# Kernel tuning notes

Measured on AMD Instinct MI355X. Metric: run time of the kernel, lower is better.

Reference implementation:

```python
import jax, jax.numpy as jnp
import numpy as np
from jax import lax

C = 128
HEADS = 4
WS = 7      # spatial search window (per side radius 3)
WT = 1      # temporal radius -> frames t-1..t+1
EPS = 1e-6

_R = WS // 2
OFFS = np.array([(dt, dh, dw)
                 for dt in range(-WT, WT + 1)
                 for dh in range(-_R, _R + 1)
                 for dw in range(-_R, _R + 1)], dtype=np.int32)  # [L,3]


def layernorm_c(x, g, b):
    # LayerNorm2D: normalize over channel dim of [B,T,C,H,W]
    mu = jnp.mean(x, axis=2, keepdims=True)
    var = jnp.var(x, axis=2, keepdims=True)
    xn = (x - mu) * lax.rsqrt(var + EPS)
    return xn * g[None, None, :, None, None] + b[None, None, :, None, None]


def conv2d(x, w, b):
    y = lax.conv_general_dilated(x, w, (1, 1), 'SAME',
                                 dimension_numbers=('NCHW', 'OIHW', 'NCHW'))
    return y + b[None, :, None, None]


def setup_inputs() -> dict:
    key = jax.random.key(0)
    ks = jax.random.split(key, 16)
    B, T, H, W = 1, 4, 128, 128
    vid = jax.random.normal(ks[0], (B, T, C, H, W), jnp.float32)
    flows = jax.random.normal(ks[1], (B, T, 2, H, W), jnp.float32)
    s = 1.0 / np.sqrt(C)
    Wq = jax.random.normal(ks[2], (C, C), jnp.float32) * s
    Wk = jax.random.normal(ks[3], (C, C), jnp.float32) * s
    Wv = jax.random.normal(ks[4], (C, C), jnp.float32) * s
    Wo = jax.random.normal(ks[5], (C, C), jnp.float32) * s
    g0 = jnp.ones((C,), jnp.float32); b0 = jnp.zeros((C,), jnp.float32)
    g1 = jnp.ones((C,), jnp.float32); b1 = jnp.zeros((C,), jnp.float32)
    sc = 1.0 / np.sqrt(C * 9)
    w_r1 = jax.random.normal(ks[6], (C, C, 3, 3), jnp.float32) * sc
    b_r1 = jnp.zeros((C,), jnp.float32)
    w_r2 = jax.random.normal(ks[7], (C, C, 3, 3), jnp.float32) * sc
    b_r2 = jnp.zeros((C,), jnp.float32)
    return dict(vid=vid, flows=flows, g0=g0, b0=b0, Wq=Wq, Wk=Wk, Wv=Wv, Wo=Wo,
                g1=g1, b1=b1, w_r1=w_r1, b_r1=b_r1, w_r2=w_r2, b_r2=b_r2)


def _forward(vid, flows, g0, b0, Wq, Wk, Wv, Wo, g1, b1, w_r1, b_r1, w_r2, b_r2):
    B, T, _, H, W = vid.shape
    hd = C // HEADS
    N = T * H * W
    scale = hd ** -0.5

    x = layernorm_c(vid, g0, b0)
    q = jnp.einsum('btchw,oc->btohw', x, Wq)
    k = jnp.einsum('btchw,oc->btohw', x, Wk)
    v = jnp.einsum('btchw,oc->btohw', x, Wv)
    qh = q.transpose(0, 1, 3, 4, 2).reshape(B, N, HEADS, hd)
    kf = k.transpose(0, 1, 3, 4, 2).reshape(B, N, C)
    vf = v.transpose(0, 1, 3, 4, 2).reshape(B, N, C)

    tt = jnp.arange(T)[:, None, None]
    hh = jnp.arange(H)[None, :, None]
    ww = jnp.arange(W)[None, None, :]
    fh = flows[:, :, 0]  # [B,T,H,W]
    fw = flows[:, :, 1]
    offs = jnp.asarray(OFFS)

    def score_body(_, off):
        dt, dh, dw = off[0], off[1], off[2]
        t_i = jnp.clip(tt + dt, 0, T - 1)                        # [T,H,W]
        oh = jnp.round(fh * dt).astype(jnp.int32)                 # flow-guided center
        ow = jnp.round(fw * dt).astype(jnp.int32)
        h_i = jnp.clip(hh[None] + oh + dh, 0, H - 1)              # [B,T,H,W]
        w_i = jnp.clip(ww[None] + ow + dw, 0, W - 1)
        flat = ((jnp.broadcast_to(t_i[None], (B, T, H, W)) * H + h_i) * W + w_i).reshape(B, N)
        kg = jnp.take_along_axis(kf, flat[:, :, None], axis=1).reshape(B, N, HEADS, hd)
        s = jnp.einsum('bnhd,bnhd->bnh', qh, kg) * scale
        return None, (s, flat)

    _, (scores, flats) = lax.scan(score_body, None, offs)         # [L,B,N,HD], [L,B,N]
    wts = jax.nn.softmax(scores, axis=0)

    def agg_body(acc, inp):
        wl, fl = inp
        vg = jnp.take_along_axis(vf, fl[:, :, None], axis=1).reshape(B, N, HEADS, hd)
        return acc + wl[..., None] * vg, None

    acc, _ = lax.scan(agg_body, jnp.zeros((B, N, HEADS, hd), vid.dtype), (wts, flats))
    attn = acc.reshape(B, T, H, W, C).transpose(0, 1, 4, 2, 3)
    attn = jnp.einsum('btchw,oc->btohw', attn, Wo)

    vid1 = vid + attn
    y = layernorm_c(vid1, g1, b1)
    yb = y.reshape(B * T, C, H, W)
    r = conv2d(yb, w_r1, b_r1)
    r = jax.nn.gelu(r)
    r = conv2d(r, w_r2, b_r2)
    res = (yb + r).reshape(B, T, C, H, W)
    return vid1 + res


def reference(vid, flows, g0, b0, Wq, Wk, Wv, Wo, g1, b1, w_r1, b_r1, w_r2, b_r2):
    return _forward(vid, flows, g0, b0, Wq, Wk, Wv, Wo, g1, b1, w_r1, b_r1, w_r2, b_r2)
```

## Files before the change

kernel.cpp:

```cpp
#include <hip/hip_runtime.h>

__device__ __forceinline__ float bflo(unsigned int u){ return __builtin_bit_cast(float, (unsigned int)(u<<16)); }
__device__ __forceinline__ float bfhi(unsigned int u){ return __builtin_bit_cast(float, (unsigned int)(u & 0xffff0000u)); }
__device__ __forceinline__ float b2f(unsigned short s){ return __builtin_bit_cast(float, ((unsigned int)s)<<16); }
__device__ __forceinline__ unsigned short f2b(float f){
  unsigned int x = __builtin_bit_cast(unsigned int, f);
  x += 0x7fffu + ((x>>16)&1u);
  return (unsigned short)(x>>16);
}
__device__ __forceinline__ unsigned int packbf(float a, float b){
  return (unsigned int)f2b(a) | ((unsigned int)f2b(b)<<16);
}
__device__ __forceinline__ unsigned short f2h(float f){
  return __builtin_bit_cast(unsigned short, (_Float16)f);
}
__device__ __forceinline__ float dpp_swap1(float s){
  int so = __builtin_amdgcn_mov_dpp(__builtin_bit_cast(int, s), 0xB1, 0xF, 0xF, true);
  return __builtin_bit_cast(float, so);
}
__device__ __forceinline__ unsigned swz(unsigned b){ return b ^ (((b>>8)&7u)<<4); }

using bf16x8 = __attribute__((ext_vector_type(8))) short;
using f32x4  = __attribute__((ext_vector_type(4))) float;
using f32x2  = __attribute__((ext_vector_type(2))) float;
using h2     = __attribute__((ext_vector_type(2))) _Float16;

__device__ __forceinline__ h2 uh(unsigned int u){ return __builtin_bit_cast(h2, u); }

#define NPOS 65536
#define SLOT_ELEMS 8388608
#define WM_OFF 6291456

__global__ __launch_bounds__(256) void k_wprep(const float* __restrict__ w1,
                                               const float* __restrict__ w2,
                                               const float* __restrict__ Wq,
                                               const float* __restrict__ Wk,
                                               const float* __restrict__ Wv,
                                               const float* __restrict__ Wo,
                                               unsigned short* __restrict__ o1,
                                               unsigned short* __restrict__ o2,
                                               unsigned short* __restrict__ wm){
  int idx = blockIdx.x*256 + threadIdx.x;
  if (idx < 147456){
    int o = idx / 1152;
    int rem = idx - o*1152;
    int c = rem / 9;
    int tap = rem - c*9;
    int dsti = tap*16384 + o*128 + c;
    o1[dsti] = f2b(w1[idx]);
    o2[dsti] = f2b(w2[idx]);
  } else if (idx < 212992){
    int idx2 = idx - 147456;
    int mat = idx2 >> 14;
    int ij  = idx2 & 16383;
    float v = (mat==0) ? Wq[ij]*0.2550348613f
            : (mat==1) ? Wk[ij]
            : (mat==2) ? Wv[ij] : Wo[ij];
    wm[idx2] = f2b(v);
  }
}

__global__ __launch_bounds__(256) void k_ln_nchw(const float* __restrict__ vid,
                                                 const float* __restrict__ g,
                                                 const float* __restrict__ b,
                                                 unsigned short* __restrict__ xf){
  int n = blockIdx.x*256 + threadIdx.x;
  int t = n >> 14, hw = n & 16383;
  const float* base = vid + (size_t)t*2097152 + hw;
  float s=0.f, ss=0.f;
  #pragma unroll 8
  for (int c=0;c<128;c++){ float v=base[(size_t)c*16384]; s+=v; ss+=v*v; }
  float mu  = s*0.0078125f;
  float var = fmaxf(ss*0.0078125f - mu*mu, 0.f);
  float rs  = rsqrtf(var + 1e-6f);
  unsigned int* op = (unsigned int*)(xf + (size_t)n*128);
  #pragma unroll 4
  for (int c=0;c<128;c+=2){
    float v0=(base[(size_t)c*16384]    -mu)*rs*g[c]  +b[c];
    float v1=(base[(size_t)(c+1)*16384]-mu)*rs*g[c+1]+b[c+1];
    op[c>>1]=packbf(v0,v1);
  }
}

__global__ __launch_bounds__(256) void k_ln_rows(const unsigned short* __restrict__ x,
                                                 const float* __restrict__ g,
                                                 const float* __restrict__ b,
                                                 unsigned short* __restrict__ y){
  int n = blockIdx.x*256 + threadIdx.x;
  const unsigned int* p = (const unsigned int*)(x + (size_t)n*128);
  float s=0.f, ss=0.f;
  #pragma unroll 8
  for (int j=0;j<64;j++){ unsigned int u=p[j]; float v0=bflo(u),v1=bfhi(u); s+=v0+v1; ss+=v0*v0+v1*v1; }
  float mu  = s*0.0078125f;
  float var = fmaxf(ss*0.0078125f - mu*mu, 0.f);
  float rs  = rsqrtf(var + 1e-6f);
  unsigned int* op=(unsigned int*)(y+(size_t)n*128);
  #pragma unroll 8
  for (int j=0;j<64;j++){
    unsigned int u=p[j];
    float v0=(bflo(u)-mu)*rs*g[2*j]  +b[2*j];
    float v1=(bfhi(u)-mu)*rs*g[2*j+1]+b[2*j+1];
    op[j]=packbf(v0,v1);
  }
}

__global__ __launch_bounds__(256) void k_qkv(const unsigned short* xf,
                                             const unsigned short* __restrict__ wm,
                                             unsigned short* qf,
                                             unsigned short* __restrict__ kfo,
                                             unsigned short* __restrict__ vfo){
  __shared__ unsigned short wlds[16384];
  int wave = threadIdx.x>>6, lane = threadIdx.x&63;
  int m0w = blockIdx.x*256 + wave*64;
  int mrow = lane&15, quad = lane>>4;
  #pragma unroll 1
  for (int mi=0; mi<3; mi++){
    int mat = 2-mi;
    __syncthreads();
    { const uint4* src=(const uint4*)(wm + mat*16384);
      #pragma unroll
      for (int i=0;i<8;i++){
        unsigned bb=(threadIdx.x+256*i)*16;
        *(uint4*)((char*)wlds + swz(bb)) = src[threadIdx.x+256*i];
      } }
    __syncthreads();
    #pragma unroll 1
    for (int mt=0; mt<4; mt++){
      int m0 = m0w + mt*16;
      bf16x8 a[4];
      const unsigned short* ap = xf + (size_t)(m0+mrow)*128 + quad*8;
      #pragma unroll
      for (int kc=0;kc<4;kc++) a[kc] = *(const bf16x8*)(ap + kc*32);
      for (int nt=0;nt<8;nt++){
        f32x4 acc = {0.f,0.f,0.f,0.f};
        #pragma unroll
        for (int kc=0;kc<4;kc++){
          bf16x8 bfr = *(const bf16x8*)((const char*)wlds + swz((nt*16+mrow)*256 + kc*64 + quad*16));
          acc = __builtin_amdgcn_mfma_f32_16x16x32_bf16(a[kc], bfr, acc, 0,0,0);
        }
        int col = nt*16+mrow;
        if (mat==2){
          unsigned char* op8 = (unsigned char*)vfo + (size_t)(m0 + quad*4)*128 + col;
          #pragma unroll
          for (int r=0;r<4;r++){
            int pk = __builtin_amdgcn_cvt_pk_fp8_f32(acc[r], acc[r], 0, false);
            op8[(size_t)r*128] = (unsigned char)(pk & 0xff);
          }
        } else {
          unsigned short* out = (mat==0) ? qf : kfo;
          unsigned short* op = out + (size_t)(m0 + quad*4)*128 + col;
          #pragma unroll
          for (int r=0;r<4;r++) op[(size_t)r*128] = f2h(acc[r]);
        }
      }
    }
  }
}

__global__ __launch_bounds__(256) void k_attn(const unsigned short* qf,
                                              const unsigned short* __restrict__ kf,
                                              const unsigned short* __restrict__ vf,
                                              const float* __restrict__ flw,
                                              unsigned short* attf){
  int xcd = blockIdx.x & 7;
  int j   = blockIdx.x >> 3;
  int t       = j >> 6;
  int r       = j & 63;
  int h_local = r >> 2;
  int wq      = r & 3;
  int h = xcd*16 + h_local;
  int w = wq*32 + (threadIdx.x >> 3);
  int head  = (threadIdx.x >> 1) & 3;
  int cpart = threadIdx.x & 1;
  int hw = (h<<7) + w;
  int n  = (t<<14) + hw;
  float fh = flw[t*32768 + hw];
  float fw = flw[t*32768 + 16384 + hw];
  unsigned coff = head*32 + cpart*16;
  const unsigned char* vf8 = (const unsigned char*)vf;
  const uint4* qp = (const uint4*)(qf + (size_t)n*128 + coff);
  uint4 q0v = qp[0], q1v = qp[1];
  unsigned qw[8] = {q0v.x,q0v.y,q0v.z,q0v.w,q1v.x,q1v.y,q1v.z,q1v.w};
  float acc[16];
  #pragma unroll
  for (int i=0;i<16;i++) acc[i]=0.f;
  float l = 0.f;

  int rowb0, rowb1, rowb2;
  int hb0, hb1, hb2;
  int wm30, wm31, wm32;
  int w0c0, w0c1, w0c2;
  {
    int ti;
    ti = t-1; ti = ti<0?0:ti;   rowb0 = ti<<14;
    rowb1 = t<<14;
    ti = t+1; ti = ti>3?3:ti;   rowb2 = ti<<14;
    int oh = (int)rintf(fh*(-1.0f)), ow = (int)rintf(fw*(-1.0f));
    hb0 = h+oh; wm30 = w+ow-3;
    hb1 = h;    wm31 = w-3;
    oh = (int)rintf(fh*(1.0f)); ow = (int)rintf(fw*(1.0f));
    hb2 = h+oh; wm32 = w+ow-3;
    w0c0 = wm30<0?0:(wm30>127?127:wm30);
    w0c1 = wm31<0?0:(wm31>127?127:wm31);
    w0c2 = wm32<0?0:(wm32>127?127:wm32);
  }

  uint4 ka0, ka1, va;
  {
    int hi0 = hb0-3; hi0 = hi0<0?0:(hi0>127?127:hi0);
    unsigned b0 = ((unsigned)(rowb0 + (hi0<<7) + w0c0)<<7) + coff;
    ka0 = ((const uint4*)(kf + b0))[0];
    ka1 = ((const uint4*)(kf + b0))[1];
    va  = *(const uint4*)(vf8 + b0);
  }

  #pragma unroll
  for (int x=0; x<3; x++){
    const int rb_t = (x==0)?rowb0:((x==1)?rowb1:rowb2);
    const int hb   = (x==0)?hb0:((x==1)?hb1:hb2);
    const int wm3  = (x==0)?wm30:((x==1)?wm31:wm32);
    const int w0c  = (x==0)?w0c0:((x==1)?w0c1:w0c2);
    const int nrb  = (x==0)?rowb1:rowb2;
    const int nhb  = (x==0)?hb1:hb2;
    const int nw0c = (x==0)?w0c1:w0c2;
    #pragma unroll 1
    for (int dh=-3; dh<=3; dh++){
      int hi = hb+dh; hi = hi<0?0:(hi>127?127:hi);
      int rbase = rb_t + (hi<<7);
      #pragma unroll
      for (int i=0;i<7;i++){
        unsigned bon;
        if (i<6){
          int wi = wm3+i+1; wi = wi<0?0:(wi>127?127:wi);
          bon = ((unsigned)(rbase + wi)<<7) + coff;
        } else if (dh<3){
          int hi2 = hb+dh+1; hi2 = hi2<0?0:(hi2>127?127:hi2);
          bon = ((unsigned)(rb_t + (hi2<<7) + w0c)<<7) + coff;
        } else if (x<2){
          int hi2 = nhb-3; hi2 = hi2<0?0:(hi2>127?127:hi2);
          bon = ((unsigned)(nrb + (hi2<<7) + nw0c)<<7) + coff;
        } else {
          bon = coff;
        }
        uint4 kb0 = ((const uint4*)(kf + bon))[0];
        uint4 kb1 = ((const uint4*)(kf + bon))[1];
        uint4 vb  = *(const uint4*)(vf8 + bon);
        float s0 = 0.f, s1 = 0.f;
        s0 = __builtin_amdgcn_fdot2(uh(qw[0]), uh(ka0.x), s0, false);
        s0 = __builtin_amdgcn_fdot2(uh(qw[1]), uh(ka0.y), s0, false);
        s0 = __builtin_amdgcn_fdot2(uh(qw[2]), uh(ka0.z), s0, false);
        s0 = __builtin_amdgcn_fdot2(uh(qw[3]), uh(ka0.w), s0, false);
        s1 = __builtin_amdgcn_fdot2(uh(qw[4]), uh(ka1.x), s1, false);
        s1 = __builtin_amdgcn_fdot2(uh(qw[5]), uh(ka1.y), s1, false);
        s1 = __builtin_amdgcn_fdot2(uh(qw[6]), uh(ka1.z), s1, false);
        s1 = __builtin_amdgcn_fdot2(uh(qw[7]), uh(ka1.w), s1, false);
        float s = s0 + s1;
        s += dpp_swap1(s);
        float e = exp2f(s);
        l += e;
        f32x2 c0 = __builtin_amdgcn_cvt_pk_f32_fp8((int)va.x, false);
        f32x2 c1 = __builtin_amdgcn_cvt_pk_f32_fp8((int)va.x, true);
        f32x2 c2 = __builtin_amdgcn_cvt_pk_f32_fp8((int)va.y, false);
        f32x2 c3 = __builtin_amdgcn_cvt_pk_f32_fp8((int)va.y, true);
        f32x2 c4 = __builtin_amdgcn_cvt_pk_f32_fp8((int)va.z, false);
        f32x2 c5 = __builtin_amdgcn_cvt_pk_f32_fp8((int)va.z, true);
        f32x2 c6 = __builtin_amdgcn_cvt_pk_f32_fp8((int)va.w, false);
        f32x2 c7 = __builtin_amdgcn_cvt_pk_f32_fp8((int)va.w, true);
        acc[0]  += e*c0.x; acc[1]  += e*c0.y;
        acc[2]  += e*c1.x; acc[3]  += e*c1.y;
        acc[4]  += e*c2.x; acc[5]  += e*c2.y;
        acc[6]  += e*c3.x; acc[7]  += e*c3.y;
        acc[8]  += e*c4.x; acc[9]  += e*c4.y;
        acc[10] += e*c5.x; acc[11] += e*c5.y;
        acc[12] += e*c6.x; acc[13] += e*c6.y;
        acc[14] += e*c7.x; acc[15] += e*c7.y;
        ka0=kb0; ka1=kb1; va=vb;
      }
    }
  }
  float inv = 1.f/l;
  unsigned int* op = (unsigned int*)(attf + (size_t)n*128 + coff);
  #pragma unroll
  for (int i=0;i<8;i++) op[i]=packbf(acc[2*i]*inv, acc[2*i+1]*inv);
}

__global__ __launch_bounds__(256) void k_wo(const unsigned short* attf,
                                            const unsigned short* __restrict__ wm,
                                            const float* __restrict__ vid,
                                            unsigned short* vid1){
  __shared__ unsigned short wlds[16384];
  int wave = threadIdx.x>>6, lane = threadIdx.x&63;
  int m0w = blockIdx.x*256 + wave*64;
  int mrow = lane&15, quad = lane>>4;
  { const uint4* src=(const uint4*)(wm + 49152);
    #pragma unroll
    for (int i=0;i<8;i++){
      unsigned bb=(threadIdx.x+256*i)*16;
      *(uint4*)((char*)wlds + swz(bb)) = src[threadIdx.x+256*i];
    } }
  __syncthreads();
  #pragma unroll 1
  for (int mt=0; mt<4; mt++){
    int m0 = m0w + mt*16;
    bf16x8 a[4];
    const unsigned short* ap = attf + (size_t)(m0+mrow)*128 + quad*8;
    #pragma unroll
    for (int kc=0;kc<4;kc++) a[kc] = *(const bf16x8*)(ap + kc*32);
    for (int nt=0;nt<8;nt++){
      f32x4 acc={0.f,0.f,0.f,0.f};
      #pragma unroll
      for (int kc=0;kc<4;kc++){
        bf16x8 bfr = *(const bf16x8*)((const char*)wlds + swz((nt*16+mrow)*256 + kc*64 + quad*16));
        acc = __builtin_amdgcn_mfma_f32_16x16x32_bf16(a[kc], bfr, acc, 0,0,0);
      }
      int col = nt*16+mrow;
      #pragma unroll
      for (int r=0;r<4;r++){
        int nrow = m0 + quad*4 + r;
        int tt = nrow>>14, hww = nrow&16383;
        float resid = vid[(size_t)tt*2097152 + (size_t)col*16384 + hww];
        vid1[(size_t)nrow*128 + col] = f2b(resid + acc[r]);
      }
    }
  }
}

#define CONV_PROLOG \
  __shared__ unsigned short wlds[8192]; \
  __shared__ unsigned short inlds[16384]; \
  int wv = threadIdx.x>>6, lane = threadIdx.x&63; \
  int mrow = lane&15, quad = lane>>4; \
  int chalf = blockIdx.x & 1; \
  int h = (blockIdx.x>>1) & 127; \
  int frame = blockIdx.x>>8; \
  size_t nf = (size_t)frame*16384; \
  f32x4 accA[4], accB[4]; \
  _Pragma("unroll") \
  for (int i=0;i<4;i++){ accA[i]=(f32x4){0.f,0.f,0.f,0.f}; accB[i]=(f32x4){0.f,0.f,0.f,0.f}; } \
  { const uint4* sp=(const uint4*)(wtap + chalf*8192); \
    uint4 s0=sp[threadIdx.x], s1=sp[threadIdx.x+256], s2=sp[threadIdx.x+512], s3=sp[threadIdx.x+768]; \
    unsigned b0=(unsigned)threadIdx.x*16; \
    *(uint4*)((char*)wlds + swz(b0))         = s0; \
    *(uint4*)((char*)wlds + swz(b0+4096u))   = s1; \
    *(uint4*)((char*)wlds + swz(b0+8192u))   = s2; \
    *(uint4*)((char*)wlds + swz(b0+12288u))  = s3; \
    if (h>=1){ const uint4* ip=(const uint4*)(src + (nf + (size_t)(h-1)*128)*128); \
      _Pragma("unroll") \
      for (int j2=0;j2<8;j2++) \
        *(uint4*)((char*)inlds + swz((unsigned)(threadIdx.x+256*j2)*16)) = ip[threadIdx.x+256*j2]; } } \
  __syncthreads(); \
  _Pragma("unroll 1") \
  for (int ky=0; ky<3; ky++){ \
    int h2c = h+ky-1; \
    bool vld = (unsigned)h2c<128u; \
    _Pragma("unroll 1") \
    for (int kx=0; kx<3; kx++){ \
      int tap = ky*3+kx; \
      uint4 s0,s1,s2,s3; \
      if (tap<8){ const uint4* sp=(const uint4*)(wtap + (size_t)(tap+1)*16384 + chalf*8192); \
        s0=sp[threadIdx.x]; s1=sp[threadIdx.x+256]; s2=sp[threadIdx.x+512]; s3=sp[threadIdx.x+768]; } \
      uint4 tr[8]; \
      bool stg = (kx==2) && (ky<2) && (h+ky<128); \
      if (stg){ const uint4* ip=(const uint4*)(src + (nf + (size_t)(h+ky)*128)*128); \
        _Pragma("unroll") \
        for (int j2=0;j2<8;j2++) tr[j2]=ip[threadIdx.x+256*j2]; } \
      if (vld){ \
        int wA = wv*32 + mrow + kx - 1;             \
        int wAc = wA < 0 ? 0 : wA; \
        int wB = wA + 16;                           \
        int wBc = wB > 127 ? 127 : wB; \
        bf16x8 aA[4], aB[4]; \
        _Pragma("unroll") \
        for (int kc=0;kc<4;kc++){ \
          aA[kc]=*(const bf16x8*)((const char*)inlds + swz((unsigned)(wAc*256 + kc*64 + quad*16))); \
          aB[kc]=*(const bf16x8*)((const char*)inlds + swz((unsigned)(wBc*256 + kc*64 + quad*16))); } \
        if (kx==0 && wv==0 && mrow==0){ _Pragma("unroll") for (int kc=0;kc<4;kc++) aA[kc]=(bf16x8){0,0,0,0,0,0,0,0}; } \
        if (kx==2 && wv==3 && mrow==15){ _Pragma("unroll") for (int kc=0;kc<4;kc++) aB[kc]=(bf16x8){0,0,0,0,0,0,0,0}; } \
        _Pragma("unroll") \
        for (int nt=0;nt<4;nt++){ \
          _Pragma("unroll") \
          for (int kc=0;kc<4;kc++){ \
            bf16x8 bfr=*(const bf16x8*)((const char*)wlds + swz((nt*16+mrow)*256 + kc*64 + quad*16)); \
            accA[nt]=__builtin_amdgcn_mfma_f32_16x16x32_bf16(aA[kc],bfr,accA[nt],0,0,0); \
            accB[nt]=__builtin_amdgcn_mfma_f32_16x16x32_bf16(aB[kc],bfr,accB[nt],0,0,0); \
          } \
        } \
      } \
      __syncthreads(); \
      if (tap<8){ unsigned b0=(unsigned)threadIdx.x*16; \
        *(uint4*)((char*)wlds + swz(b0))         = s0; \
        *(uint4*)((char*)wlds + swz(b0+4096u))   = s1; \
        *(uint4*)((char*)wlds + swz(b0+8192u))   = s2; \
        *(uint4*)((char*)wlds + swz(b0+12288u))  = s3; } \
      if (stg){ \
        _Pragma("unroll") \
        for (int j2=0;j2<8;j2++) \
          *(uint4*)((char*)inlds + swz((unsigned)(threadIdx.x+256*j2)*16)) = tr[j2]; } \
      if (tap<8) __syncthreads(); \
    } \
  }

__global__ __launch_bounds__(256) void k_conv_gelu(const unsigned short* __restrict__ src,
                                                   const unsigned short* __restrict__ wtap,
                                                   const float* __restrict__ bias,
                                                   unsigned short* __restrict__ dst){
  CONV_PROLOG
  #pragma unroll
  for (int nt=0;nt<4;nt++){
    int col = chalf*64 + nt*16 + mrow;
    float bb = bias[col];
    #pragma unroll
    for (int r=0;r<4;r++){
      int pA = h*128 + wv*32 + quad*4 + r;
      float xA = accA[nt][r]+bb;
      float zA = 0.7978845608028654f*(xA+0.044715f*xA*xA*xA);
      dst[(nf+(size_t)pA)*128+col] = f2b(xA * __builtin_amdgcn_rcpf(1.f + __expf(-2.f*zA)));
      float xB = accB[nt][r]+bb;
      float zB = 0.7978845608028654f*(xB+0.044715f*xB*xB*xB);
      dst[(nf+(size_t)(pA+16))*128+col] = f2b(xB * __builtin_amdgcn_rcpf(1.f + __expf(-2.f*zB)));
    }
  }
}

__global__ __launch_bounds__(256) void k_conv_final(const unsigned short* __restrict__ src,
                                                    const unsigned short* __restrict__ wtap,
                                                    const float* __restrict__ bias,
                                                    const unsigned short* __restrict__ yb,
                                                    const unsigned short* __restrict__ vid1,
                                                    float* __restrict__ out){
  CONV_PROLOG
  #pragma unroll
  for (int nt=0;nt<4;nt++){
    int col = chalf*64 + nt*16 + mrow;
    float bb = bias[col];
    #pragma unroll
    for (int r=0;r<4;r++){
      int pA = h*128 + wv*32 + quad*4 + r;
      size_t rowA = nf+(size_t)pA, rowB = rowA+16;
      float xA = accA[nt][r]+bb;
      out[(size_t)frame*2097152 + (size_t)col*16384 + pA] =
        b2f(vid1[rowA*128+col]) + b2f(yb[rowA*128+col]) + xA;
      float xB = accB[nt][r]+bb;
      out[(size_t)frame*2097152 + (size_t)col*16384 + pA + 16] =
        b2f(vid1[rowB*128+col]) + b2f(yb[rowB*128+col]) + xB;
    }
  }
}

extern "C" void kernel_launch(void* const* d_in, const int* in_sizes, int n_in,
                              void* d_out, int out_size, void* d_ws, size_t ws_size,
                              hipStream_t stream) {
  const float* vid  = (const float*)d_in[0];
  const float* flw  = (const float*)d_in[1];
  const float* g0   = (const float*)d_in[2];
  const float* b0   = (const float*)d_in[3];
  const float* Wq   = (const float*)d_in[4];
  const float* Wk   = (const float*)d_in[5];
  const float* Wv   = (const float*)d_in[6];
  const float* Wo   = (const float*)d_in[7];
  const float* g1   = (const float*)d_in[8];
  const float* b1   = (const float*)d_in[9];
  const float* wr1  = (const float*)d_in[10];
  const float* br1  = (const float*)d_in[11];
  const float* wr2  = (const float*)d_in[12];
  const float* br2  = (const float*)d_in[13];
  float* out = (float*)d_out;

  unsigned short* A  = (unsigned short*)d_ws;
  unsigned short* Bs = A + SLOT_ELEMS;
  unsigned short* Cs = Bs + SLOT_ELEMS;
  bool four = ws_size >= (size_t)4*SLOT_ELEMS*2 + 2*294912;
  unsigned short* D  = four ? (Cs + SLOT_ELEMS) : A;
  unsigned short* wt1 = Cs + SLOT_ELEMS + (four ? SLOT_ELEMS : 0);
  unsigned short* wt2 = wt1 + 147456;
  unsigned short* wm  = Cs + WM_OFF;

  k_wprep   <<<832, 256, 0, stream>>>(wr1, wr2, Wq, Wk, Wv, Wo, wt1, wt2, wm);
  k_ln_nchw <<<256, 256, 0, stream>>>(vid, g0, b0, A);
  k_qkv     <<<256, 256, 0, stream>>>(A, wm, D, Bs, Cs);
  k_attn    <<<2048,256, 0, stream>>>(D, Bs, Cs, flw, D);
  k_wo      <<<256, 256, 0, stream>>>(D, wm, vid, D);
  k_ln_rows <<<256, 256, 0, stream>>>(D, g1, b1, Bs);
  k_conv_gelu <<<1024,256,0, stream>>>(Bs, wt1, br1, Cs);
  k_conv_final<<<1024,256,0, stream>>>(Cs, wt2, br2, Bs, D, out);
}
```

Baseline: 434.8 us.

## Fuse second LayerNorm into Wo epilogue, split QKV grid, remap conv blocks

```diff
diff --git a/kernel.cpp b/kernel.cpp
--- a/kernel.cpp
+++ b/kernel.cpp
@@ -82,28 +82,6 @@
   }
 }
 
-__global__ __launch_bounds__(256) void k_ln_rows(const unsigned short* __restrict__ x,
-                                                 const float* __restrict__ g,
-                                                 const float* __restrict__ b,
-                                                 unsigned short* __restrict__ y){
-  int n = blockIdx.x*256 + threadIdx.x;
-  const unsigned int* p = (const unsigned int*)(x + (size_t)n*128);
-  float s=0.f, ss=0.f;
-  #pragma unroll 8
-  for (int j=0;j<64;j++){ unsigned int u=p[j]; float v0=bflo(u),v1=bfhi(u); s+=v0+v1; ss+=v0*v0+v1*v1; }
-  float mu  = s*0.0078125f;
-  float var = fmaxf(ss*0.0078125f - mu*mu, 0.f);
-  float rs  = rsqrtf(var + 1e-6f);
-  unsigned int* op=(unsigned int*)(y+(size_t)n*128);
-  #pragma unroll 8
-  for (int j=0;j<64;j++){
-    unsigned int u=p[j];
-    float v0=(bflo(u)-mu)*rs*g[2*j]  +b[2*j];
-    float v1=(bfhi(u)-mu)*rs*g[2*j+1]+b[2*j+1];
-    op[j]=packbf(v0,v1);
-  }
-}
-
 __global__ __launch_bounds__(256) void k_qkv(const unsigned short* xf,
                                              const unsigned short* __restrict__ wm,
                                              unsigned short* qf,
@@ -111,7 +89,7 @@
                                              unsigned short* __restrict__ vfo){
   __shared__ unsigned short wlds[16384];
   int wave = threadIdx.x>>6, lane = threadIdx.x&63;
-  int m0w = blockIdx.x*256 + wave*64;
+  int m0w = blockIdx.x*128 + wave*32;
   int mrow = lane&15, quad = lane>>4;
   #pragma unroll 1
   for (int mi=0; mi<3; mi++){
@@ -125,7 +103,7 @@
       } }
     __syncthreads();
     #pragma unroll 1
-    for (int mt=0; mt<4; mt++){
+    for (int mt=0; mt<2; mt++){
       int m0 = m0w + mt*16;
       bf16x8 a[4];
       const unsigned short* ap = xf + (size_t)(m0+mrow)*128 + quad*8;
@@ -287,7 +265,10 @@
 __global__ __launch_bounds__(256) void k_wo(const unsigned short* attf,
                                             const unsigned short* __restrict__ wm,
                                             const float* __restrict__ vid,
-                                            unsigned short* vid1){
+                                            const float* __restrict__ g1,
+                                            const float* __restrict__ b1,
+                                            unsigned short* vid1,
+                                            unsigned short* __restrict__ yb){
   __shared__ unsigned short wlds[16384];
   int wave = threadIdx.x>>6, lane = threadIdx.x&63;
   int m0w = blockIdx.x*256 + wave*64;
@@ -306,6 +287,8 @@
     const unsigned short* ap = attf + (size_t)(m0+mrow)*128 + quad*8;
     #pragma unroll
     for (int kc=0;kc<4;kc++) a[kc] = *(const bf16x8*)(ap + kc*32);
+    f32x4 acc8[8];
+    #pragma unroll
     for (int nt=0;nt<8;nt++){
       f32x4 acc={0.f,0.f,0.f,0.f};
       #pragma unroll
@@ -313,13 +296,35 @@
         bf16x8 bfr = *(const bf16x8*)((const char*)wlds + swz((nt*16+mrow)*256 + kc*64 + quad*16));
         acc = __builtin_amdgcn_mfma_f32_16x16x32_bf16(a[kc], bfr, acc, 0,0,0);
       }
-      int col = nt*16+mrow;
-      #pragma unroll
-      for (int r=0;r<4;r++){
-        int nrow = m0 + quad*4 + r;
-        int tt = nrow>>14, hww = nrow&16383;
-        float resid = vid[(size_t)tt*2097152 + (size_t)col*16384 + hww];
-        vid1[(size_t)nrow*128 + col] = f2b(resid + acc[r]);
+      acc8[nt]=acc;
+    }
+    #pragma unroll
+    for (int r=0;r<4;r++){
+      int nrow = m0 + quad*4 + r;
+      int tt = nrow>>14, hww = nrow&16383;
+      float v0,v1,v2,v3,v4,v5,v6,v7;
+      float s=0.f, ss=0.f;
+      v0 = vid[(size_t)tt*2097152 + (size_t)(0*16+mrow)*16384 + hww] + acc8[0][r];
+      v1 = vid[(size_t)tt*2097152 + (size_t)(1*16+mrow)*16384 + hww] + acc8[1][r];
+      v2 = vid[(size_t)tt*2097152 + (size_t)(2*16+mrow)*16384 + hww] + acc8[2][r];
+      v3 = vid[(size_t)tt*2097152 + (size_t)(3*16+mrow)*16384 + hww] + acc8[3][r];
+      v4 = vid[(size_t)tt*2097152 + (size_t)(4*16+mrow)*16384 + hww] + acc8[4][r];
+      v5 = vid[(size_t)tt*2097152 + (size_t)(5*16+mrow)*16384 + hww] + acc8[5][r];
+      v6 = vid[(size_t)tt*2097152 + (size_t)(6*16+mrow)*16384 + hww] + acc8[6][r];
+      v7 = vid[(size_t)tt*2097152 + (size_t)(7*16+mrow)*16384 + hww] + acc8[7][r];
+      s  = ((v0+v1)+(v2+v3)) + ((v4+v5)+(v6+v7));
+      ss = ((v0*v0+v1*v1)+(v2*v2+v3*v3)) + ((v4*v4+v5*v5)+(v6*v6+v7*v7));
+      #pragma unroll
+      for (int m=1;m<16;m<<=1){ s += __shfl_xor(s,m,64); ss += __shfl_xor(ss,m,64); }
+      float mu  = s*0.0078125f;
+      float var = fmaxf(ss*0.0078125f - mu*mu, 0.f);
+      float rs  = rsqrtf(var + 1e-6f);
+      float vv[8] = {v0,v1,v2,v3,v4,v5,v6,v7};
+      #pragma unroll
+      for (int nt=0;nt<8;nt++){
+        int col = nt*16+mrow;
+        vid1[(size_t)nrow*128 + col] = f2b(vv[nt]);
+        yb[(size_t)nrow*128 + col]   = f2b((vv[nt]-mu)*rs*g1[col] + b1[col]);
       }
     }
   }
@@ -330,9 +335,10 @@
   __shared__ unsigned short inlds[16384]; \
   int wv = threadIdx.x>>6, lane = threadIdx.x&63; \
   int mrow = lane&15, quad = lane>>4; \
-  int chalf = blockIdx.x & 1; \
-  int h = (blockIdx.x>>1) & 127; \
-  int frame = blockIdx.x>>8; \
+  int wg = (int)((blockIdx.x&7)*128 + (blockIdx.x>>3));    \
+  int chalf = wg & 1; \
+  int h = (wg>>1) & 127; \
+  int frame = wg>>8; \
   size_t nf = (size_t)frame*16384; \
   f32x4 accA[4], accB[4]; \
   _Pragma("unroll") \
@@ -477,10 +483,9 @@
 
   k_wprep   <<<832, 256, 0, stream>>>(wr1, wr2, Wq, Wk, Wv, Wo, wt1, wt2, wm);
   k_ln_nchw <<<256, 256, 0, stream>>>(vid, g0, b0, A);
-  k_qkv     <<<256, 256, 0, stream>>>(A, wm, D, Bs, Cs);
+  k_qkv     <<<512, 256, 0, stream>>>(A, wm, D, Bs, Cs);
   k_attn    <<<2048,256, 0, stream>>>(D, Bs, Cs, flw, D);
-  k_wo      <<<256, 256, 0, stream>>>(D, wm, vid, D);
-  k_ln_rows <<<256, 256, 0, stream>>>(D, g1, b1, Bs);
+  k_wo      <<<256, 256, 0, stream>>>(D, wm, vid, g1, b1, D, Bs);
   k_conv_gelu <<<1024,256,0, stream>>>(Bs, wt1, br1, Cs);
   k_conv_final<<<1024,256,0, stream>>>(Cs, wt2, br2, Bs, D, out);
 }
```

After: 429.2 us. About the same (-1.3%).
